# Kernel optimization log

Hardware: AMD Instinct MI355X
Metric: run time of the kernel (lower is better)

## Reference

```python
import jax, jax.numpy as jnp
import numpy as np

HEADS = 16
DIM_HEAD = 64
RMS_EPS = 1.1920929e-07  # torch.finfo(float32).eps (torch RMSNorm eps=None default)
ROPE_THETA = 10000.0


def _rope(x):
    # x: [b, h, n, d]; rotary-embedding-torch style interleaved rotation
    n, d = x.shape[-2], x.shape[-1]
    inv_freq = 1.0 / (ROPE_THETA ** (jnp.arange(0, d, 2, dtype=jnp.float32) / d))
    t = jnp.arange(n, dtype=jnp.float32)
    freqs = t[:, None] * inv_freq[None, :]              # [n, d/2]
    cos = jnp.repeat(jnp.cos(freqs), 2, axis=-1)        # [n, d] interleaved
    sin = jnp.repeat(jnp.sin(freqs), 2, axis=-1)
    x1 = x[..., ::2]
    x2 = x[..., 1::2]
    rot = jnp.stack((-x2, x1), axis=-1).reshape(x.shape)  # rotate_half, interleaved pairs
    return x * cos + rot * sin


def setup_inputs() -> dict:
    key = jax.random.key(0)
    ks = jax.random.split(key, 6)
    b, n, dim = 2, 2048, 1024
    tokens = jax.random.normal(ks[0], (b, n, dim), dtype=jnp.float32)
    norm_weight = jnp.ones((dim,), dtype=jnp.float32)
    wq = jax.random.normal(ks[1], (dim, dim), dtype=jnp.float32) * 0.02
    wk = jax.random.normal(ks[2], (dim, dim), dtype=jnp.float32) * 0.02
    wv = jax.random.normal(ks[3], (dim, dim), dtype=jnp.float32) * 0.02
    wo = jax.random.normal(ks[4], (dim, dim), dtype=jnp.float32) * 0.02
    return {"tokens": tokens, "norm_weight": norm_weight, "wq": wq, "wk": wk, "wv": wv, "wo": wo}


def reference(tokens, norm_weight, wq, wk, wv, wo):
    b, n, dim = tokens.shape
    # RMSNorm (elementwise affine)
    x = tokens * jax.lax.rsqrt(jnp.mean(tokens * tokens, axis=-1, keepdims=True) + RMS_EPS)
    x = x * norm_weight
    # QKV projections (torch Linear: x @ W.T), split heads: b n (h d) -> b h n d
    def split(y):
        return y.reshape(b, n, HEADS, DIM_HEAD).transpose(0, 2, 1, 3)
    q = split(x @ wq.T) * (DIM_HEAD ** -0.5)
    k = split(x @ wk.T)
    v = split(x @ wv.T)
    # rotary embedding (no kv cache -> same positions for q and k)
    q = _rope(q)
    k = _rope(k)
    sim = jnp.einsum('bhid,bhjd->bhij', q, k)
    causal = jnp.triu(jnp.ones((n, n), dtype=bool), k=1)
    sim = jnp.where(causal, -jnp.finfo(sim.dtype).max, sim)
    attn = jax.nn.softmax(sim, axis=-1)
    out = jnp.einsum('bhij,bhjd->bhid', attn, v)
    out = out.transpose(0, 2, 1, 3).reshape(b, n, dim)  # merge heads
    return out @ wo.T
```

## Files before the change

### kernel.cpp

```cpp
#include <hip/hip_runtime.h>

typedef __bf16 bf16x8 __attribute__((ext_vector_type(8)));
typedef float f32x4 __attribute__((ext_vector_type(4)));

#define DIM 1024
#define NSEQ 2048

#define GL2LDS(g, l) __builtin_amdgcn_global_load_lds( \
    (const __attribute__((address_space(1))) void*)(g), \
    (__attribute__((address_space(3))) void*)(l), 16, 0, 0)

__global__ __launch_bounds__(256) void cvt_kernel(const float* __restrict__ s,
                                                  __bf16* __restrict__ d) {
    int i = (blockIdx.x * 256 + threadIdx.x) * 4;
    float4 f = *(const float4*)(s + i);
    union { uint2 u; __bf16 h[4]; } p;
    p.h[0] = (__bf16)f.x; p.h[1] = (__bf16)f.y;
    p.h[2] = (__bf16)f.z; p.h[3] = (__bf16)f.w;
    *(uint2*)(d + i) = p.u;
}

__global__ void init_kernel(int* c) { c[threadIdx.x] = 0; }

__global__ __launch_bounds__(256) void rmsnorm_kernel(const float* __restrict__ x,
                                                      const float* __restrict__ g,
                                                      __bf16* __restrict__ o) {
    int row = blockIdx.x;
    int t = threadIdx.x;
    float4 xv = ((const float4*)(x + (size_t)row * DIM))[t];
    float ss = xv.x*xv.x + xv.y*xv.y + xv.z*xv.z + xv.w*xv.w;
    #pragma unroll
    for (int off = 32; off; off >>= 1) ss += __shfl_xor(ss, off, 64);
    __shared__ float red[4];
    if ((t & 63) == 0) red[t >> 6] = ss;
    __syncthreads();
    ss = red[0] + red[1] + red[2] + red[3];
    float r = rsqrtf(ss * (1.0f / 1024.0f) + 1.1920929e-07f);
    float4 gv = ((const float4*)g)[t];
    union { uint2 u; __bf16 h[4]; } p;
    p.h[0] = (__bf16)(xv.x * r * gv.x);
    p.h[1] = (__bf16)(xv.y * r * gv.y);
    p.h[2] = (__bf16)(xv.z * r * gv.z);
    p.h[3] = (__bf16)(xv.w * r * gv.w);
    *(uint2*)(o + (size_t)row * DIM + t * 4) = p.u;
}

__global__ __launch_bounds__(256) void rope_kernel(__bf16* __restrict__ x) {
    int gid = blockIdx.x * 256 + threadIdx.x;
    int row = gid >> 9;
    int pr = gid & 511;
    int pos = row & (NSEQ - 1);
    int dp = pr & 31;
    float inv = __expf(-(float)dp * (9.210340371976184f / 32.0f));
    float ang = (float)pos * inv;
    float sn, cs;
    sincosf(ang, &sn, &cs);
    size_t off = (size_t)row * DIM + pr * 2;
    union { unsigned int u; __bf16 h[2]; } p;
    p.u = *(const unsigned int*)(x + off);
    float x1 = (float)p.h[0], x2 = (float)p.h[1];
    p.h[0] = (__bf16)(x1 * cs - x2 * sn);
    p.h[1] = (__bf16)(x2 * cs + x1 * sn);
    *(unsigned int*)(x + off) = p.u;
}

template <typename CT>
__device__ __forceinline__ void gemm_body(const __bf16* __restrict__ A,
                                          const __bf16* __restrict__ B,
                                          CT* __restrict__ C,
                                          int mb, int nb, int ldc, float scale,
                                          __bf16* As, __bf16* Bs) {
    int t = threadIdx.x;
    int w = t >> 6, l = t & 63;
    int wm = (w >> 1) * 64, wn = (w & 1) * 64;
    int lrow = l & 15, lq = l >> 4;
    f32x4 acc[4][4] = {};

    int srow = w * 32 + (l >> 3);
    int sc8 = (l & 7) * 8;
    const __bf16* gA = A + (size_t)(mb * 128 + srow) * 1024 + sc8;
    const __bf16* gB = B + (size_t)(nb * 128 + srow) * 1024 + sc8;
    __bf16* lA = As + (size_t)(w * 32) * 64;
    __bf16* lB = Bs + (size_t)(w * 32) * 64;

    for (int kt = 0; kt < 16; ++kt) {
        int k0 = kt * 64;
        #pragma unroll
        for (int c = 0; c < 4; ++c) {
            GL2LDS(gA + (size_t)c * 8 * 1024 + k0, lA + c * 8 * 64);
            GL2LDS(gB + (size_t)c * 8 * 1024 + k0, lB + c * 8 * 64);
        }
        __syncthreads();
        #pragma unroll
        for (int ch = 0; ch < 2; ++ch) {
            bf16x8 af[4], bfr[4];
            #pragma unroll
            for (int i = 0; i < 4; ++i)
                af[i] = *(const bf16x8*)&As[(wm + i * 16 + lrow) * 64 + ch * 32 + lq * 8];
            #pragma unroll
            for (int i = 0; i < 4; ++i)
                bfr[i] = *(const bf16x8*)&Bs[(wn + i * 16 + lrow) * 64 + ch * 32 + lq * 8];
            #pragma unroll
            for (int rt = 0; rt < 4; ++rt)
                #pragma unroll
                for (int ct = 0; ct < 4; ++ct)
                    acc[rt][ct] = __builtin_amdgcn_mfma_f32_16x16x32_bf16(
                        af[rt], bfr[ct], acc[rt][ct], 0, 0, 0);
        }
        __syncthreads();
    }
    #pragma unroll
    for (int rt = 0; rt < 4; ++rt)
        #pragma unroll
        for (int ct = 0; ct < 4; ++ct)
            #pragma unroll
            for (int r = 0; r < 4; ++r) {
                int row = mb * 128 + wm + rt * 16 + lq * 4 + r;
                int col = nb * 128 + wn + ct * 16 + lrow;
                C[(size_t)row * ldc + col] = (CT)(acc[rt][ct][r] * scale);
            }
}

__global__ __launch_bounds__(256) void qkv_kernel(const __bf16* __restrict__ x,
                                                  const __bf16* __restrict__ wq,
                                                  const __bf16* __restrict__ wk,
                                                  const __bf16* __restrict__ wv,
                                                  __bf16* __restrict__ qb,
                                                  __bf16* __restrict__ kb,
                                                  __bf16* __restrict__ vtb) {
    __shared__ __bf16 As[128 * 64];
    __shared__ __bf16 Bs[128 * 64];
    int bm = blockIdx.x, bn = blockIdx.y, z = blockIdx.z;
    if (z == 0)      gemm_body<__bf16>(x,  wq, qb,  bm, bn, 1024, 0.125f, As, Bs);
    else if (z == 1) gemm_body<__bf16>(x,  wk, kb,  bm, bn, 1024, 1.0f,   As, Bs);
    else             gemm_body<__bf16>(wv, x,  vtb, bn, bm, 4096, 1.0f,   As, Bs);
}

__global__ __launch_bounds__(256) void wo_kernel(const __bf16* __restrict__ A,
                                                 const __bf16* __restrict__ B,
                                                 float* __restrict__ C) {
    __shared__ __bf16 As[128 * 64];
    __shared__ __bf16 Bs[128 * 64];
    gemm_body<float>(A, B, C, blockIdx.x, blockIdx.y, 1024, 1.0f, As, Bs);
}

__global__ __launch_bounds__(256, 2) void attn_kernel(const __bf16* __restrict__ q,
                                                      const __bf16* __restrict__ kk,
                                                      const __bf16* __restrict__ vt,
                                                      __bf16* __restrict__ o,
                                                      int* __restrict__ counters) {
    int xcd = blockIdx.x & 7;
    int t = threadIdx.x;
    int w = t >> 6, l = t & 63;
    int lrow = l & 15, lq = l >> 4;
    int row0 = t >> 3;
    int c8 = (t & 7) * 8;

    __shared__ __bf16 Kt[2][64 * 72];
    __shared__ __bf16 Vs[2][64 * 72];
    __shared__ __bf16 Ps[4 * 16 * 72];
    __shared__ int s_item;
    __bf16* pw = &Ps[w * 16 * 72];

    for (;;) {
        if (t == 0) s_item = atomicAdd(&counters[xcd], 1);
        __syncthreads();
        int item = s_item;
        if (item >= 128) break;
        int qt = 31 - (item >> 2);
        int bh = xcd * 4 + (item & 3);
        int h = bh & 15;
        int b = bh >> 4;
        int rowbase = b * NSEQ;

        const __bf16* kbase = kk + (size_t)rowbase * DIM + h * 64;
        const __bf16* vbase = vt + (size_t)(h * 64) * 4096 + b * 2048;

        const __bf16* qp = q + (size_t)(rowbase + qt * 64 + w * 16 + lrow) * DIM + h * 64;
        bf16x8 qb0 = *(const bf16x8*)(qp + lq * 8);
        bf16x8 qb1 = *(const bf16x8*)(qp + 32 + lq * 8);

        f32x4 oacc[4] = {};
        float m_r = -1e30f, l_r = 0.0f;

        uint4 kr0, kr1, vr0, vr1;
        kr0 = *(const uint4*)(kbase + (size_t)row0 * DIM + c8);
        kr1 = *(const uint4*)(kbase + (size_t)(row0 + 32) * DIM + c8);
        vr0 = *(const uint4*)(vbase + (size_t)row0 * 4096 + c8);
        vr1 = *(const uint4*)(vbase + (size_t)(row0 + 32) * 4096 + c8);
        *(uint4*)&Kt[0][row0 * 72 + c8] = kr0;
        *(uint4*)&Kt[0][(row0 + 32) * 72 + c8] = kr1;
        *(uint4*)&Vs[0][row0 * 72 + c8] = vr0;
        *(uint4*)&Vs[0][(row0 + 32) * 72 + c8] = vr1;
        __syncthreads();

        for (int jt = 0; jt <= qt; ++jt) {
            int cur = jt & 1;
            if (jt < qt) {
                int j0 = (jt + 1) * 64;
                kr0 = *(const uint4*)(kbase + (size_t)(j0 + row0) * DIM + c8);
                kr1 = *(const uint4*)(kbase + (size_t)(j0 + row0 + 32) * DIM + c8);
                vr0 = *(const uint4*)(vbase + (size_t)row0 * 4096 + j0 + c8);
                vr1 = *(const uint4*)(vbase + (size_t)(row0 + 32) * 4096 + j0 + c8);
            }
            f32x4 st[4];
            #pragma unroll
            for (int ct = 0; ct < 4; ++ct) {
                f32x4 z = {};
                bf16x8 ka0 = *(const bf16x8*)&Kt[cur][(ct * 16 + lrow) * 72 + lq * 8];
                bf16x8 ka1 = *(const bf16x8*)&Kt[cur][(ct * 16 + lrow) * 72 + 32 + lq * 8];
                z = __builtin_amdgcn_mfma_f32_16x16x32_bf16(ka0, qb0, z, 0, 0, 0);
                z = __builtin_amdgcn_mfma_f32_16x16x32_bf16(ka1, qb1, z, 0, 0, 0);
                st[ct] = z;
            }
            if (jt == qt) {
                int qr = w * 16 + lrow;
                #pragma unroll
                for (int ct = 0; ct < 4; ++ct)
                    #pragma unroll
                    for (int r = 0; r < 4; ++r)
                        if (ct * 16 + lq * 4 + r > qr) st[ct][r] = -3.0e38f;
            }
            float mx = st[0][0];
            #pragma unroll
            for (int ct = 0; ct < 4; ++ct)
                #pragma unroll
                for (int r = 0; r < 4; ++r) mx = fmaxf(mx, st[ct][r]);
            mx = fmaxf(mx, __shfl_xor(mx, 16, 64));
            mx = fmaxf(mx, __shfl_xor(mx, 32, 64));
            float mnew = fmaxf(m_r, mx);
            float alpha = __expf(m_r - mnew);
            float ps = 0.0f;
            #pragma unroll
            for (int ct = 0; ct < 4; ++ct)
                #pragma unroll
                for (int r = 0; r < 4; ++r) {
                    float p = __expf(st[ct][r] - mnew);
                    st[ct][r] = p;
                    ps += p;
                }
            ps += __shfl_xor(ps, 16, 64);
            ps += __shfl_xor(ps, 32, 64);
            l_r = l_r * alpha + ps;
            m_r = mnew;

            #pragma unroll
            for (int ct = 0; ct < 4; ++ct) {
                union { uint2 u; __bf16 h4[4]; } pk;
                #pragma unroll
                for (int r = 0; r < 4; ++r) pk.h4[r] = (__bf16)st[ct][r];
                *(uint2*)&pw[lrow * 72 + ct * 16 + lq * 4] = pk.u;
            }
            #pragma unroll
            for (int ct = 0; ct < 4; ++ct)
                #pragma unroll
                for (int r = 0; r < 4; ++r) oacc[ct][r] *= alpha;
            bf16x8 pb0 = *(const bf16x8*)&pw[lrow * 72 + lq * 8];
            bf16x8 pb1 = *(const bf16x8*)&pw[lrow * 72 + 32 + lq * 8];
            #pragma unroll
            for (int ct = 0; ct < 4; ++ct) {
                bf16x8 va0 = *(const bf16x8*)&Vs[cur][(ct * 16 + lrow) * 72 + lq * 8];
                bf16x8 va1 = *(const bf16x8*)&Vs[cur][(ct * 16 + lrow) * 72 + 32 + lq * 8];
                oacc[ct] = __builtin_amdgcn_mfma_f32_16x16x32_bf16(va0, pb0, oacc[ct], 0, 0, 0);
                oacc[ct] = __builtin_amdgcn_mfma_f32_16x16x32_bf16(va1, pb1, oacc[ct], 0, 0, 0);
            }
            if (jt < qt) {
                *(uint4*)&Kt[cur ^ 1][row0 * 72 + c8] = kr0;
                *(uint4*)&Kt[cur ^ 1][(row0 + 32) * 72 + c8] = kr1;
                *(uint4*)&Vs[cur ^ 1][row0 * 72 + c8] = vr0;
                *(uint4*)&Vs[cur ^ 1][(row0 + 32) * 72 + c8] = vr1;
            }
            __syncthreads();
        }
        float rcp = 1.0f / l_r;
        const size_t orow = (size_t)(rowbase + qt * 64 + w * 16 + lrow) * DIM + h * 64;
        #pragma unroll
        for (int ct = 0; ct < 4; ++ct) {
            union { uint2 u; __bf16 h4[4]; } pk;
            #pragma unroll
            for (int r = 0; r < 4; ++r) pk.h4[r] = (__bf16)(oacc[ct][r] * rcp);
            *(uint2*)(o + orow + ct * 16 + lq * 4) = pk.u;
        }
    }
}

extern "C" void kernel_launch(void* const* d_in, const int* in_sizes, int n_in,
                              void* d_out, int out_size, void* d_ws, size_t ws_size,
                              hipStream_t stream) {
    const float* tokens = (const float*)d_in[0];
    const float* gamma  = (const float*)d_in[1];
    const float* wq = (const float*)d_in[2];
    const float* wk = (const float*)d_in[3];
    const float* wv = (const float*)d_in[4];
    const float* wo = (const float*)d_in[5];

    __bf16* ws  = (__bf16*)d_ws;
    __bf16* x   = ws;
    __bf16* qb  = x   + (size_t)4096 * 1024;
    __bf16* kb  = qb  + (size_t)4096 * 1024;
    __bf16* vtb = kb  + (size_t)4096 * 1024;
    __bf16* ao  = x;
    __bf16* wob = qb;
    float*  out = (float*)d_out;

    __bf16* wqb = (__bf16*)d_out;
    __bf16* wkb = wqb + (size_t)1024 * 1024;
    __bf16* wvb = wkb + (size_t)1024 * 1024;
    int* counters = (int*)((char*)d_out + (size_t)8 * 1024 * 1024);

    cvt_kernel<<<1024, 256, 0, stream>>>(wq, wqb);
    cvt_kernel<<<1024, 256, 0, stream>>>(wk, wkb);
    cvt_kernel<<<1024, 256, 0, stream>>>(wv, wvb);

    rmsnorm_kernel<<<4096, 256, 0, stream>>>(tokens, gamma, x);

    qkv_kernel<<<dim3(32, 8, 3), 256, 0, stream>>>(x, wqb, wkb, wvb, qb, kb, vtb);

    rope_kernel<<<8192, 256, 0, stream>>>(qb);
    rope_kernel<<<8192, 256, 0, stream>>>(kb);

    init_kernel<<<1, 8, 0, stream>>>(counters);

    attn_kernel<<<512, 256, 0, stream>>>(qb, kb, vtb, ao, counters);

    cvt_kernel<<<1024, 256, 0, stream>>>(wo, wob);

    wo_kernel<<<dim3(32, 8), 256, 0, stream>>>(ao, wob, out);
}
```

Before: 213.6 us.

## Merge small launches, use exp2 softmax with lazy rescale, raise attention occupancy

Fuses the three weight conversions and the counter init into one launch, and merges the two rope launches into one. Folds log2(e) into the Q scale so the softmax uses the hardware exp2, and skips the running-max rescale of the accumulator unless the max grows by more than a threshold. Raises attention occupancy to three blocks per CU and launches more persistent blocks. This cuts launch overhead and VALU work in the inner loop, but the lazy rescale lets exponentials reach up to 2^8 before correction, and the tighter register budget may cause spills.

```diff
diff --git a/kernel.cpp b/kernel.cpp
--- a/kernel.cpp
+++ b/kernel.cpp
@@ -20,7 +20,24 @@
     *(uint2*)(d + i) = p.u;
 }
 
-__global__ void init_kernel(int* c) { c[threadIdx.x] = 0; }
+__global__ __launch_bounds__(256) void cvt3_kernel(const float* __restrict__ wq,
+                                                   const float* __restrict__ wk,
+                                                   const float* __restrict__ wv,
+                                                   __bf16* __restrict__ dq,
+                                                   __bf16* __restrict__ dk,
+                                                   __bf16* __restrict__ dv,
+                                                   int* __restrict__ counters) {
+    if (blockIdx.x == 0 && blockIdx.y == 0 && threadIdx.x < 8)
+        counters[threadIdx.x] = 0;
+    const float* s = blockIdx.y == 0 ? wq : (blockIdx.y == 1 ? wk : wv);
+    __bf16*      d = blockIdx.y == 0 ? dq : (blockIdx.y == 1 ? dk : dv);
+    int i = (blockIdx.x * 256 + threadIdx.x) * 4;
+    float4 f = *(const float4*)(s + i);
+    union { uint2 u; __bf16 h[4]; } p;
+    p.h[0] = (__bf16)f.x; p.h[1] = (__bf16)f.y;
+    p.h[2] = (__bf16)f.z; p.h[3] = (__bf16)f.w;
+    *(uint2*)(d + i) = p.u;
+}
 
 __global__ __launch_bounds__(256) void rmsnorm_kernel(const float* __restrict__ x,
                                                       const float* __restrict__ g,
@@ -45,8 +62,11 @@
     *(uint2*)(o + (size_t)row * DIM + t * 4) = p.u;
 }
 
-__global__ __launch_bounds__(256) void rope_kernel(__bf16* __restrict__ x) {
-    int gid = blockIdx.x * 256 + threadIdx.x;
+__global__ __launch_bounds__(256) void rope_kernel(__bf16* __restrict__ qb,
+                                                   __bf16* __restrict__ kb) {
+    int bid = blockIdx.x;
+    __bf16* x = (bid & 1) ? kb : qb;
+    int gid = (bid >> 1) * 256 + threadIdx.x;
     int row = gid >> 9;
     int pr = gid & 511;
     int pos = row & (NSEQ - 1);
@@ -131,7 +151,8 @@
     __shared__ __bf16 As[128 * 64];
     __shared__ __bf16 Bs[128 * 64];
     int bm = blockIdx.x, bn = blockIdx.y, z = blockIdx.z;
-    if (z == 0)      gemm_body<__bf16>(x,  wq, qb,  bm, bn, 1024, 0.125f, As, Bs);
+    if (z == 0)      gemm_body<__bf16>(x,  wq, qb,  bm, bn, 1024,
+                                       0.125f * 1.44269504088896340736f, As, Bs);
     else if (z == 1) gemm_body<__bf16>(x,  wk, kb,  bm, bn, 1024, 1.0f,   As, Bs);
     else             gemm_body<__bf16>(wv, x,  vtb, bn, bm, 4096, 1.0f,   As, Bs);
 }
@@ -144,7 +165,7 @@
     gemm_body<float>(A, B, C, blockIdx.x, blockIdx.y, 1024, 1.0f, As, Bs);
 }
 
-__global__ __launch_bounds__(256, 2) void attn_kernel(const __bf16* __restrict__ q,
+__global__ __launch_bounds__(256, 3) void attn_kernel(const __bf16* __restrict__ q,
                                                       const __bf16* __restrict__ kk,
                                                       const __bf16* __restrict__ vt,
                                                       __bf16* __restrict__ o,
@@ -228,21 +249,28 @@
                 for (int r = 0; r < 4; ++r) mx = fmaxf(mx, st[ct][r]);
             mx = fmaxf(mx, __shfl_xor(mx, 16, 64));
             mx = fmaxf(mx, __shfl_xor(mx, 32, 64));
-            float mnew = fmaxf(m_r, mx);
-            float alpha = __expf(m_r - mnew);
+            if (!__all(mx - m_r <= 8.0f)) {
+                float mnew = fmaxf(m_r, mx);
+                float alpha = __builtin_amdgcn_exp2f(m_r - mnew);
+                l_r *= alpha;
+                #pragma unroll
+                for (int ct = 0; ct < 4; ++ct)
+                    #pragma unroll
+                    for (int r = 0; r < 4; ++r) oacc[ct][r] *= alpha;
+                m_r = mnew;
+            }
             float ps = 0.0f;
             #pragma unroll
             for (int ct = 0; ct < 4; ++ct)
                 #pragma unroll
                 for (int r = 0; r < 4; ++r) {
-                    float p = __expf(st[ct][r] - mnew);
+                    float p = __builtin_amdgcn_exp2f(st[ct][r] - m_r);
                     st[ct][r] = p;
                     ps += p;
                 }
             ps += __shfl_xor(ps, 16, 64);
             ps += __shfl_xor(ps, 32, 64);
-            l_r = l_r * alpha + ps;
-            m_r = mnew;
+            l_r += ps;
 
             #pragma unroll
             for (int ct = 0; ct < 4; ++ct) {
@@ -251,10 +279,6 @@
                 for (int r = 0; r < 4; ++r) pk.h4[r] = (__bf16)st[ct][r];
                 *(uint2*)&pw[lrow * 72 + ct * 16 + lq * 4] = pk.u;
             }
-            #pragma unroll
-            for (int ct = 0; ct < 4; ++ct)
-                #pragma unroll
-                for (int r = 0; r < 4; ++r) oacc[ct][r] *= alpha;
             bf16x8 pb0 = *(const bf16x8*)&pw[lrow * 72 + lq * 8];
             bf16x8 pb1 = *(const bf16x8*)&pw[lrow * 72 + 32 + lq * 8];
             #pragma unroll
@@ -308,20 +332,15 @@
     __bf16* wvb = wkb + (size_t)1024 * 1024;
     int* counters = (int*)((char*)d_out + (size_t)8 * 1024 * 1024);
 
-    cvt_kernel<<<1024, 256, 0, stream>>>(wq, wqb);
-    cvt_kernel<<<1024, 256, 0, stream>>>(wk, wkb);
-    cvt_kernel<<<1024, 256, 0, stream>>>(wv, wvb);
+    cvt3_kernel<<<dim3(1024, 3), 256, 0, stream>>>(wq, wk, wv, wqb, wkb, wvb, counters);
 
     rmsnorm_kernel<<<4096, 256, 0, stream>>>(tokens, gamma, x);
 
     qkv_kernel<<<dim3(32, 8, 3), 256, 0, stream>>>(x, wqb, wkb, wvb, qb, kb, vtb);
 
-    rope_kernel<<<8192, 256, 0, stream>>>(qb);
-    rope_kernel<<<8192, 256, 0, stream>>>(kb);
-
-    init_kernel<<<1, 8, 0, stream>>>(counters);
-
-    attn_kernel<<<512, 256, 0, stream>>>(qb, kb, vtb, ao, counters);
+    rope_kernel<<<16384, 256, 0, stream>>>(qb, kb);
+
+    attn_kernel<<<768, 256, 0, stream>>>(qb, kb, vtb, ao, counters);
 
     cvt_kernel<<<1024, 256, 0, stream>>>(wo, wob);
 
```

After: 206.2 us. 1.04x faster.
